# Kernel optimization log

Hardware: AMD Instinct MI355X
Metric: run time of the kernel (lower is better)

Reference implementation:

```python
import jax, jax.numpy as jnp
import numpy as np
import math

NUM_EXPERTS = 8
CAP_FACTOR = 1.25
MIN_CAPACITY = 4

def _capacity(num_tokens, num_experts):
    cap = math.floor(CAP_FACTOR * num_tokens / num_experts)
    cap += cap % 2
    return max(cap, MIN_CAPACITY)

def setup_inputs() -> dict:
    key = jax.random.key(0)
    k1, k2, k3, k4 = jax.random.split(key, 4)
    tokens, d_model, d_ff, E = 8192, 1024, 4096, NUM_EXPERTS
    x = jax.random.normal(k1, (tokens, d_model), dtype=jnp.float32)
    gate_weight = jax.random.normal(k2, (E, d_model), dtype=jnp.float32) * math.sqrt(0.1 / d_model)
    expert_weight = jax.random.normal(k3, (E, d_model, d_ff), dtype=jnp.float32) * 0.02
    expert_bias = jax.random.normal(k4, (E, 1, d_ff), dtype=jnp.float32) * 0.02
    return {"x": x, "gate_weight": gate_weight, "expert_weight": expert_weight, "expert_bias": expert_bias}

def reference(x, gate_weight, expert_weight, expert_bias):
    tokens, d_model = x.shape
    E = gate_weight.shape[0]
    capacity = _capacity(tokens, E)
    # FP32 gate (Switch-style)
    gate_logits = jnp.dot(x.astype(jnp.float32), gate_weight.astype(jnp.float32).T)  # [s, E]
    logits = jax.nn.softmax(gate_logits, axis=-1)  # auto_cast_softmax in fp32
    # Top-1 routing, select_policy='first'
    top1_idx = jnp.argmax(gate_logits, axis=-1)  # argmax over raw gate output
    mask = jax.nn.one_hot(top1_idx, E, dtype=jnp.int32)  # [s, E]
    # aux load-balancing loss (training path)
    me = jnp.mean(logits, axis=0)
    ce = jnp.mean(mask.astype(jnp.float32), axis=0)
    l_aux = E * jnp.sum(me * ce)
    # cumsum-based capacity ranking
    ranks = jnp.cumsum(mask, axis=0) - 1  # [s, E]
    mask = mask * (ranks < capacity).astype(jnp.int32)
    ranks_tok = jnp.sum(mask * ranks, axis=-1)  # [s]
    rank_oh = jax.nn.one_hot(ranks_tok, capacity, dtype=logits.dtype)  # [s, c]
    weight = mask.astype(logits.dtype) * logits  # [s, E]
    combine_weights = weight[:, :, None] * rank_oh[:, None, :]  # [s, E, c]
    sec_mask = combine_weights != 0  # bool dispatch mask
    # scatter dispatch: [s,E,c] x [s,d] -> [E,c,d]
    dispatched = jnp.einsum("sec,sd->ecd", sec_mask.astype(x.dtype), x)
    # per-expert front linear: [E,c,d] x [E,d,f] -> [E,c,f]
    out = jnp.einsum("ecd,edf->ecf", dispatched, expert_weight) + expert_bias
    return out, combine_weights, l_aux
```

## Files before the change

kernel.cpp:

```cpp
#include <hip/hip_runtime.h>
#include <hip/hip_bf16.h>

#define TOKENS 8192
#define DM 1024
#define DFF 4096
#define NE 8
#define CAP 1280
#define ECAP (NE*CAP)
#define OUT_ELEMS ((size_t)NE*CAP*DFF)
#define CMB_ELEMS ((size_t)TOKENS*NE*CAP)
#define ZROW TOKENS
#define GBK 32

typedef __attribute__((ext_vector_type(8))) short short8;
typedef __attribute__((ext_vector_type(16))) float f32x16;
typedef __attribute__((ext_vector_type(4))) float f4;

__device__ inline ushort f2bf(float f) {
    __hip_bfloat16 h = __float2bfloat16(f);
    return *reinterpret_cast<ushort*>(&h);
}

__device__ __forceinline__ void gload16(const ushort* g, short* l) {
    __builtin_amdgcn_global_load_lds(
        (const __attribute__((address_space(1))) void*)g,
        (__attribute__((address_space(3))) void*)l, 16, 0, 0);
}

__global__ __launch_bounds__(256) void gate_kernel(const float* __restrict__ x,
        const float* __restrict__ gw, float* __restrict__ probs8, int* __restrict__ top1,
        ushort* __restrict__ xbf) {
    int wave = threadIdx.x >> 6;
    int lane = threadIdx.x & 63;
    int t = blockIdx.x * 4 + wave;
    const float* xrow = x + (size_t)t * DM;
    float4 xv[4];
    #pragma unroll
    for (int j = 0; j < 4; ++j) xv[j] = *(const float4*)(xrow + lane * 4 + j * 256);
    ushort* xbrow = xbf + (size_t)t * DM;
    #pragma unroll
    for (int j = 0; j < 4; ++j) {
        ushort4 o;
        o.x = f2bf(xv[j].x); o.y = f2bf(xv[j].y); o.z = f2bf(xv[j].z); o.w = f2bf(xv[j].w);
        *(ushort4*)(xbrow + lane * 4 + j * 256) = o;
    }
    float logit[8];
    #pragma unroll
    for (int e = 0; e < 8; ++e) {
        const float* g = gw + e * DM;
        float s = 0.f;
        #pragma unroll
        for (int j = 0; j < 4; ++j) {
            float4 gv = *(const float4*)(g + lane * 4 + j * 256);
            s += xv[j].x * gv.x + xv[j].y * gv.y + xv[j].z * gv.z + xv[j].w * gv.w;
        }
        #pragma unroll
        for (int off = 32; off >= 1; off >>= 1) s += __shfl_xor(s, off);
        logit[e] = s;
    }
    if (lane == 0) {
        int bi = 0; float bv = logit[0];
        #pragma unroll
        for (int e = 1; e < 8; ++e) if (logit[e] > bv) { bv = logit[e]; bi = e; }
        float se = 0.f, p[8];
        #pragma unroll
        for (int e = 0; e < 8; ++e) { p[e] = expf(logit[e] - bv); se += p[e]; }
        float inv = 1.f / se;
        #pragma unroll
        for (int e = 0; e < 8; ++e) probs8[t * 8 + e] = p[e] * inv;
        top1[t] = bi;
    }
    if (blockIdx.x == 0) {
        ushort4 z; z.x = z.y = z.z = z.w = 0;
        *(ushort4*)(xbf + (size_t)ZROW * DM + threadIdx.x * 4) = z;
    }
}

__global__ __launch_bounds__(512) void cvtw_rank_kernel(
        const float* __restrict__ w, ushort* __restrict__ wt,
        const int* __restrict__ top1, const float* __restrict__ probs8,
        int* __restrict__ slot_token, int* __restrict__ pos,
        int* __restrict__ cnts, float* __restrict__ laux_out) {
    __shared__ __align__(16) char smem[TOKENS * 4 + 64 * 4 + 8 * 4];
    const int tid = threadIdx.x;
    if (blockIdx.x == 0) {
        int* t1s = (int*)smem;
        float* red = (float*)(smem + TOKENS * 4);
        int* cnt_sh = (int*)(smem + TOKENS * 4 + 64 * 4);
        int w8 = tid >> 6;
        int lane = tid & 63;
        for (int i = tid; i < TOKENS; i += 512) t1s[i] = top1[i];
        for (int i = tid; i < ECAP; i += 512) slot_token[i] = ZROW;
        for (int i = tid; i < TOKENS; i += 512) pos[i] = -1;

        float ps[8];
        #pragma unroll
        for (int e = 0; e < 8; ++e) ps[e] = 0.f;
        for (int t = tid; t < TOKENS; t += 512) {
            float4 a = *(const float4*)(probs8 + t * 8);
            float4 b = *(const float4*)(probs8 + t * 8 + 4);
            ps[0] += a.x; ps[1] += a.y; ps[2] += a.z; ps[3] += a.w;
            ps[4] += b.x; ps[5] += b.y; ps[6] += b.z; ps[7] += b.w;
        }
        #pragma unroll
        for (int e = 0; e < 8; ++e) {
            #pragma unroll
            for (int off = 32; off >= 1; off >>= 1) ps[e] += __shfl_xor(ps[e], off);
        }
        if (lane == 0) {
            #pragma unroll
            for (int e = 0; e < 8; ++e) red[w8 * 8 + e] = ps[e];
        }
        __syncthreads();

        int base = 0;
        for (int t0 = 0; t0 < TOKENS; t0 += 256) {
            #pragma unroll
            for (int q = 0; q < 4; ++q) {
                int t = t0 + q * 64 + lane;
                bool mine = (t1s[t] == w8);
                unsigned long long m = __ballot(mine);
                if (mine) {
                    int r = base + __popcll(m & ((1ull << lane) - 1ull));
                    if (r < CAP) { slot_token[w8 * CAP + r] = t; pos[t] = w8 * CAP + r; }
                }
                base += __popcll(m);
            }
        }
        if (lane == 0) { cnt_sh[w8] = base; cnts[w8] = (base < CAP) ? base : CAP; }
        __syncthreads();
        if (tid == 0) {
            float la = 0.f;
            #pragma unroll
            for (int e = 0; e < 8; ++e) {
                float me = 0.f;
                #pragma unroll
                for (int wv = 0; wv < 8; ++wv) me += red[wv * 8 + e];
                la += (me / (float)TOKENS) * ((float)cnt_sh[e] / (float)TOKENS);
            }
            laux_out[0] = la * (float)NE;
        }
        return;
    }
    float (*tile)[65] = (float(*)[65])smem;
    int b = blockIdx.x - 1;
    int e = b >> 11;
    int rem = b & 2047;
    int n0 = (rem & 63) * 64;
    int k0 = (rem >> 6) * 32;
    const float* we = w + (size_t)e * DM * DFF;
    int c = tid & 63, r0 = tid >> 6;
    #pragma unroll
    for (int i = 0; i < 4; ++i) {
        int r = r0 + i * 8;
        tile[r][c] = we[(size_t)(k0 + r) * DFF + n0 + c];
    }
    __syncthreads();
    ushort* wte = wt + (size_t)e * DFF * DM;
    int kc = tid & 31, nr0 = tid >> 5;
    #pragma unroll
    for (int i = 0; i < 4; ++i) {
        int nr = nr0 + i * 16;
        wte[(size_t)(n0 + nr) * DM + k0 + kc] = f2bf(tile[kc][nr]);
    }
}

__global__ __launch_bounds__(1024, 4) void gemm_kernel(
    const ushort* __restrict__ xbf,
    const ushort* __restrict__ wt,
    const float*  __restrict__ bias,
    const int*    __restrict__ slot_token,
    const int*    __restrict__ cnts,
    float* __restrict__ out,
    const int*    __restrict__ pos,
    const float*  __restrict__ probs8,
    float* __restrict__ cmb,
    int do_combine)
{
    const int bid = blockIdx.x;
    const int e   = bid & 7;
    const int rem = bid >> 3;
    const int nt  = rem & 15;
    const int mt  = rem >> 4;
    __shared__ __align__(16) short lds[4][16384];
    const int tid  = threadIdx.x;
    const int lane = tid & 63;
    const int wave = tid >> 6;
    const int wr = wave >> 2;
    const int wc = wave & 3;
    const int ln31 = lane & 31, lh = lane >> 5;
    const int tbeg = bid * 16;
    const bool has_cmb = do_combine && (bid < 512);

    float* orow = out + ((size_t)(e * CAP + mt * 256)) * DFF + (size_t)nt * 256;

    if (mt * 256 >= cnts[e]) {
        int c4 = tid & 63;
        int r0b = tid >> 6;
        f4 bv4 = *(const f4*)(bias + e * DFF + nt * 256 + c4 * 4);
        for (int r = r0b; r < 256; r += 16)
            __builtin_nontemporal_store(bv4, (f4*)(orow + (size_t)r * DFF + c4 * 4));
        if (has_cmb) {
            for (int i = 0; i < 16; ++i) {
                int tok = tbeg + i;
                int p = pos[tok];
                int ee = (p < 0) ? 0 : (p / CAP);
                float val = probs8[tok * 8 + ee];
                f4* row = (f4*)(cmb + (size_t)tok * ECAP);
                #pragma unroll
                for (int k = 0; k < 3; ++k) {
                    int c = tid + k * 1024;
                    if (c < ECAP / 4) {
                        int b4 = c * 4;
                        f4 v;
                        v.x = (b4 + 0 == p) ? val : 0.f;
                        v.y = (b4 + 1 == p) ? val : 0.f;
                        v.z = (b4 + 2 == p) ? val : 0.f;
                        v.w = (b4 + 3 == p) ? val : 0.f;
                        __builtin_nontemporal_store(v, row + c);
                    }
                }
            }
        }
        return;
    }

    const int r0 = tid >> 2;
    const int kg = (tid & 3) ^ ((tid >> 3) & 3);
    const int tokA = slot_token[e * CAP + mt * 256 + r0];
    const ushort* aptr = xbf + (size_t)tokA * DM + kg * 8;
    const ushort* bptr = wt + ((size_t)e * DFF + (size_t)nt * 256 + r0) * DM + kg * 8;

    #define STAGE(T) do { \
        short* base_ = &lds[(T) & 3][0]; \
        size_t ko_ = (size_t)(T) * GBK; \
        gload16(aptr + ko_, base_ + tid * 8); \
        gload16(bptr + ko_, base_ + 8192 + tid * 8); \
    } while (0)

    int aoff[4], boff[4];
    #pragma unroll
    for (int s = 0; s < 2; ++s) {
        #pragma unroll
        for (int mi = 0; mi < 2; ++mi) {
            int r = wr * 64 + mi * 32 + ln31;
            int c = lh + 2 * s;
            aoff[s * 2 + mi] = (r * 4 + (c ^ ((r >> 1) & 3))) * 8;
        }
        #pragma unroll
        for (int ni = 0; ni < 2; ++ni) {
            int rn = wc * 64 + ni * 32 + ln31;
            int c = lh + 2 * s;
            boff[s * 2 + ni] = 8192 + (rn * 4 + (c ^ ((rn >> 1) & 3))) * 8;
        }
    }

    f4* cmb_p = (f4*)cmb + (size_t)tbeg * (ECAP / 4);
    int kpart = 0, ntok = 0;
    int cur_p = -1, nxt_p = -1;
    float cur_val = 0.f, nxt_val = 0.f;
    if (has_cmb) {
        cur_p = pos[tbeg];
        { int ee = (cur_p < 0) ? 0 : (cur_p / CAP); cur_val = probs8[tbeg * 8 + ee]; }
        nxt_p = pos[tbeg + 1];
        { int ee = (nxt_p < 0) ? 0 : (nxt_p / CAP); nxt_val = probs8[(tbeg + 1) * 8 + ee]; }
    }
    #define CSTORE() do { if (has_cmb) { \
        int c_ = tid + kpart * 1024; \
        if (c_ < ECAP / 4) { \
            int b4_ = c_ * 4; \
            f4 v_; \
            v_.x = (b4_ + 0 == cur_p) ? cur_val : 0.f; \
            v_.y = (b4_ + 1 == cur_p) ? cur_val : 0.f; \
            v_.z = (b4_ + 2 == cur_p) ? cur_val : 0.f; \
            v_.w = (b4_ + 3 == cur_p) ? cur_val : 0.f; \
            __builtin_nontemporal_store(v_, cmb_p + c_); \
        } \
        if (++kpart == 3) { \
            kpart = 0; cmb_p += ECAP / 4; ++ntok; \
            cur_p = nxt_p; cur_val = nxt_val; \
            if (ntok + 1 < 16) { \
                nxt_p = pos[tbeg + ntok + 1]; \
                int ee_ = (nxt_p < 0) ? 0 : (nxt_p / CAP); \
                nxt_val = probs8[(tbeg + ntok + 1) * 8 + ee_]; \
            } \
        } \
    } } while (0)

    f32x16 acc[2][2];
    #pragma unroll
    for (int mi = 0; mi < 2; ++mi)
        #pragma unroll
        for (int ni = 0; ni < 2; ++ni)
            acc[mi][ni] = (f32x16)(0.f);

    STAGE(0); STAGE(1); STAGE(2);
    for (int t = 0; t < 32; ++t) {
        if (t < 29) {
            STAGE(t + 3);
            asm volatile("s_waitcnt vmcnt(6)" ::: "memory");
        } else if (t == 29) {
            asm volatile("s_waitcnt vmcnt(4)" ::: "memory");
        } else if (t == 30) {
            asm volatile("s_waitcnt vmcnt(2)" ::: "memory");
        } else {
            asm volatile("s_waitcnt vmcnt(0)" ::: "memory");
        }
        __builtin_amdgcn_s_barrier();
        __builtin_amdgcn_sched_barrier(0);

        const short* L = &lds[t & 3][0];
        __builtin_amdgcn_s_setprio(1);
        #pragma unroll
        for (int s = 0; s < 2; ++s) {
            short8 af[2], bfr[2];
            #pragma unroll
            for (int ni = 0; ni < 2; ++ni) bfr[ni] = *(const short8*)(L + boff[s * 2 + ni]);
            #pragma unroll
            for (int mi = 0; mi < 2; ++mi) af[mi] = *(const short8*)(L + aoff[s * 2 + mi]);
            #pragma unroll
            for (int mi = 0; mi < 2; ++mi)
                #pragma unroll
                for (int ni = 0; ni < 2; ++ni)
                    acc[mi][ni] = __builtin_amdgcn_mfma_f32_32x32x16_bf16(af[mi], bfr[ni], acc[mi][ni], 0, 0, 0);
        }
        __builtin_amdgcn_s_setprio(0);
        CSTORE();
        if (t < 16) CSTORE();
        __builtin_amdgcn_sched_barrier(0);
        asm volatile("" ::: "memory");
        __builtin_amdgcn_s_barrier();
        asm volatile("" ::: "memory");
    }
    #undef STAGE
    #undef CSTORE

    #pragma unroll
    for (int ni = 0; ni < 2; ++ni) {
        int c = wc * 64 + ni * 32 + ln31;
        float bv = bias[e * DFF + nt * 256 + c];
        #pragma unroll
        for (int mi = 0; mi < 2; ++mi) {
            #pragma unroll
            for (int reg = 0; reg < 16; ++reg) {
                int r = wr * 64 + mi * 32 + (reg & 3) + 8 * (reg >> 2) + 4 * lh;
                __builtin_nontemporal_store(acc[mi][ni][reg] + bv,
                    orow + (size_t)r * DFF + c);
            }
        }
    }
}

__global__ __launch_bounds__(256) void combine_kernel(const int* __restrict__ pos,
        const float* __restrict__ probs8, float* __restrict__ cmb) {
    int tok = blockIdx.x;
    int p = pos[tok];
    int e = p / CAP;
    float val = probs8[tok * 8 + (e < 0 ? 0 : e)];
    f4* row = (f4*)(cmb + (size_t)tok * ECAP);
    #pragma unroll
    for (int k = 0; k < 10; ++k) {
        int c = threadIdx.x + k * 256;
        int b4 = c * 4;
        f4 v;
        v.x = (b4 + 0 == p) ? val : 0.f;
        v.y = (b4 + 1 == p) ? val : 0.f;
        v.z = (b4 + 2 == p) ? val : 0.f;
        v.w = (b4 + 3 == p) ? val : 0.f;
        __builtin_nontemporal_store(v, row + c);
    }
}

extern "C" void kernel_launch(void* const* d_in, const int* in_sizes, int n_in,
                              void* d_out, int out_size, void* d_ws, size_t ws_size,
                              hipStream_t stream) {
    const float* x  = (const float*)d_in[0];
    const float* gw = (const float*)d_in[1];
    const float* ew = (const float*)d_in[2];
    const float* eb = (const float*)d_in[3];

    float* out = (float*)d_out;
    float* cmb = out + OUT_ELEMS;
    float* laux_out = cmb + CMB_ELEMS;

    float* probs8 = (float*)d_ws;
    int* top1 = (int*)(probs8 + TOKENS * 8);
    int* slot_token = top1 + TOKENS;
    int* pos = slot_token + ECAP;
    int* cnts = pos + TOKENS;

    const size_t SMALL = 1 << 20;
    const size_t WT_ELEMS_ = (size_t)NE * DFF * DM;
    const size_t XBF_ELEMS_ = (size_t)(TOKENS + 1) * DM;
    bool big_ws = ws_size >= SMALL + (WT_ELEMS_ + XBF_ELEMS_) * sizeof(ushort);
    ushort* wtbf = big_ws ? (ushort*)((char*)d_ws + SMALL) : (ushort*)cmb;
    ushort* xbf  = wtbf + WT_ELEMS_;

    gate_kernel<<<TOKENS / 4, 256, 0, stream>>>(x, gw, probs8, top1, xbf);
    cvtw_rank_kernel<<<16385, 512, 0, stream>>>(ew, wtbf, top1, probs8,
                                                slot_token, pos, cnts, laux_out);
    if (big_ws) {
        gemm_kernel<<<640, 1024, 0, stream>>>(xbf, wtbf, eb, slot_token, cnts, out,
                                              pos, probs8, cmb, 1);
    } else {
        gemm_kernel<<<640, 1024, 0, stream>>>(xbf, wtbf, eb, slot_token, cnts, out,
                                              pos, probs8, cmb, 0);
        combine_kernel<<<TOKENS, 256, 0, stream>>>(pos, probs8, cmb);
    }
}
```

Baseline: 191.5 us.

## Switch GEMM to 256x128 tiles with 512-thread blocks and triple-buffered LDS

The expert GEMM now uses 256x128 output tiles computed by 8 waves in 512-thread blocks, launched as 1280 blocks instead of 640 blocks of 1024 threads with 256x256 tiles. The LDS pipeline drops from four buffers of 32 KB to three of 24 KB, with prefetch depth 2 and separate vmcnt schedules for blocks that also write the combine tensor. Each block now writes 8 combine rows spread across the K loop and epilogue, and empty-expert tiles reuse the same store macro. This aims to improve occupancy and load balance, at the cost of lower B-tile reuse per block and more A-row loads overall.

```diff
diff --git a/kernel.cpp b/kernel.cpp
--- a/kernel.cpp
+++ b/kernel.cpp
@@ -165,7 +165,7 @@
     }
 }
 
-__global__ __launch_bounds__(1024, 4) void gemm_kernel(
+__global__ __launch_bounds__(512, 4) void gemm_kernel(
     const ushort* __restrict__ xbf,
     const ushort* __restrict__ wt,
     const float*  __restrict__ bias,
@@ -180,80 +180,19 @@
     const int bid = blockIdx.x;
     const int e   = bid & 7;
     const int rem = bid >> 3;
-    const int nt  = rem & 15;
-    const int mt  = rem >> 4;
-    __shared__ __align__(16) short lds[4][16384];
+    const int nt  = rem & 31;
+    const int mt  = rem >> 5;
+    __shared__ __align__(16) short lds[3][12288];
     const int tid  = threadIdx.x;
     const int lane = tid & 63;
     const int wave = tid >> 6;
-    const int wr = wave >> 2;
-    const int wc = wave & 3;
+    const int wr = wave >> 1;
+    const int wc = wave & 1;
     const int ln31 = lane & 31, lh = lane >> 5;
-    const int tbeg = bid * 16;
-    const bool has_cmb = do_combine && (bid < 512);
-
-    float* orow = out + ((size_t)(e * CAP + mt * 256)) * DFF + (size_t)nt * 256;
-
-    if (mt * 256 >= cnts[e]) {
-        int c4 = tid & 63;
-        int r0b = tid >> 6;
-        f4 bv4 = *(const f4*)(bias + e * DFF + nt * 256 + c4 * 4);
-        for (int r = r0b; r < 256; r += 16)
-            __builtin_nontemporal_store(bv4, (f4*)(orow + (size_t)r * DFF + c4 * 4));
-        if (has_cmb) {
-            for (int i = 0; i < 16; ++i) {
-                int tok = tbeg + i;
-                int p = pos[tok];
-                int ee = (p < 0) ? 0 : (p / CAP);
-                float val = probs8[tok * 8 + ee];
-                f4* row = (f4*)(cmb + (size_t)tok * ECAP);
-                #pragma unroll
-                for (int k = 0; k < 3; ++k) {
-                    int c = tid + k * 1024;
-                    if (c < ECAP / 4) {
-                        int b4 = c * 4;
-                        f4 v;
-                        v.x = (b4 + 0 == p) ? val : 0.f;
-                        v.y = (b4 + 1 == p) ? val : 0.f;
-                        v.z = (b4 + 2 == p) ? val : 0.f;
-                        v.w = (b4 + 3 == p) ? val : 0.f;
-                        __builtin_nontemporal_store(v, row + c);
-                    }
-                }
-            }
-        }
-        return;
-    }
-
-    const int r0 = tid >> 2;
-    const int kg = (tid & 3) ^ ((tid >> 3) & 3);
-    const int tokA = slot_token[e * CAP + mt * 256 + r0];
-    const ushort* aptr = xbf + (size_t)tokA * DM + kg * 8;
-    const ushort* bptr = wt + ((size_t)e * DFF + (size_t)nt * 256 + r0) * DM + kg * 8;
-
-    #define STAGE(T) do { \
-        short* base_ = &lds[(T) & 3][0]; \
-        size_t ko_ = (size_t)(T) * GBK; \
-        gload16(aptr + ko_, base_ + tid * 8); \
-        gload16(bptr + ko_, base_ + 8192 + tid * 8); \
-    } while (0)
-
-    int aoff[4], boff[4];
-    #pragma unroll
-    for (int s = 0; s < 2; ++s) {
-        #pragma unroll
-        for (int mi = 0; mi < 2; ++mi) {
-            int r = wr * 64 + mi * 32 + ln31;
-            int c = lh + 2 * s;
-            aoff[s * 2 + mi] = (r * 4 + (c ^ ((r >> 1) & 3))) * 8;
-        }
-        #pragma unroll
-        for (int ni = 0; ni < 2; ++ni) {
-            int rn = wc * 64 + ni * 32 + ln31;
-            int c = lh + 2 * s;
-            boff[s * 2 + ni] = 8192 + (rn * 4 + (c ^ ((rn >> 1) & 3))) * 8;
-        }
-    }
+    const int tbeg = bid * 8;
+    const bool has_cmb = do_combine && (bid < 1024);
+
+    float* orow = out + ((size_t)(e * CAP + mt * 256)) * DFF + (size_t)nt * 128;
 
     f4* cmb_p = (f4*)cmb + (size_t)tbeg * (ECAP / 4);
     int kpart = 0, ntok = 0;
@@ -265,27 +204,68 @@
         nxt_p = pos[tbeg + 1];
         { int ee = (nxt_p < 0) ? 0 : (nxt_p / CAP); nxt_val = probs8[(tbeg + 1) * 8 + ee]; }
     }
-    #define CSTORE() do { if (has_cmb) { \
-        int c_ = tid + kpart * 1024; \
-        if (c_ < ECAP / 4) { \
-            int b4_ = c_ * 4; \
-            f4 v_; \
-            v_.x = (b4_ + 0 == cur_p) ? cur_val : 0.f; \
-            v_.y = (b4_ + 1 == cur_p) ? cur_val : 0.f; \
-            v_.z = (b4_ + 2 == cur_p) ? cur_val : 0.f; \
-            v_.w = (b4_ + 3 == cur_p) ? cur_val : 0.f; \
-            __builtin_nontemporal_store(v_, cmb_p + c_); \
-        } \
-        if (++kpart == 3) { \
+    #define CSTORE() do { \
+        int c_ = tid + kpart * 512; \
+        int b4_ = c_ * 4; \
+        f4 v_; \
+        v_.x = (b4_ + 0 == cur_p) ? cur_val : 0.f; \
+        v_.y = (b4_ + 1 == cur_p) ? cur_val : 0.f; \
+        v_.z = (b4_ + 2 == cur_p) ? cur_val : 0.f; \
+        v_.w = (b4_ + 3 == cur_p) ? cur_val : 0.f; \
+        __builtin_nontemporal_store(v_, cmb_p + c_); \
+        if (++kpart == 5) { \
             kpart = 0; cmb_p += ECAP / 4; ++ntok; \
             cur_p = nxt_p; cur_val = nxt_val; \
-            if (ntok + 1 < 16) { \
+            if (ntok + 1 < 8) { \
                 nxt_p = pos[tbeg + ntok + 1]; \
                 int ee_ = (nxt_p < 0) ? 0 : (nxt_p / CAP); \
                 nxt_val = probs8[(tbeg + ntok + 1) * 8 + ee_]; \
             } \
         } \
-    } } while (0)
+    } while (0)
+
+    if (mt * 256 >= cnts[e]) {
+        int c4 = tid & 31;
+        int r0b = tid >> 5;
+        f4 bv4 = *(const f4*)(bias + e * DFF + nt * 128 + c4 * 4);
+        for (int r = r0b; r < 256; r += 16)
+            __builtin_nontemporal_store(bv4, (f4*)(orow + (size_t)r * DFF + c4 * 4));
+        if (has_cmb) { while (ntok < 8) CSTORE(); }
+        return;
+    }
+
+    const int r0a = tid >> 2;
+    const int kg = (tid & 3) ^ ((tid >> 3) & 3);
+    const int tokA0 = slot_token[e * CAP + mt * 256 + r0a];
+    const int tokA1 = slot_token[e * CAP + mt * 256 + 128 + r0a];
+    const ushort* aptr0 = xbf + (size_t)tokA0 * DM + kg * 8;
+    const ushort* aptr1 = xbf + (size_t)tokA1 * DM + kg * 8;
+    const ushort* bptr  = wt + ((size_t)e * DFF + (size_t)nt * 128 + r0a) * DM + kg * 8;
+
+    #define STAGE(T, BUF) do { \
+        short* base_ = &lds[BUF][0]; \
+        size_t ko_ = (size_t)(T) * GBK; \
+        gload16(aptr0 + ko_, base_ + tid * 8); \
+        gload16(aptr1 + ko_, base_ + 4096 + tid * 8); \
+        gload16(bptr  + ko_, base_ + 8192 + tid * 8); \
+    } while (0)
+
+    int aoff[4], boff[4];
+    #pragma unroll
+    for (int s = 0; s < 2; ++s) {
+        #pragma unroll
+        for (int mi = 0; mi < 2; ++mi) {
+            int r = wr * 64 + mi * 32 + ln31;
+            int c = lh + 2 * s;
+            aoff[s * 2 + mi] = (r * 4 + (c ^ ((r >> 1) & 3))) * 8;
+        }
+        #pragma unroll
+        for (int ni = 0; ni < 2; ++ni) {
+            int rn = wc * 64 + ni * 32 + ln31;
+            int c = lh + 2 * s;
+            boff[s * 2 + ni] = 8192 + (rn * 4 + (c ^ ((rn >> 1) & 3))) * 8;
+        }
+    }
 
     f32x16 acc[2][2];
     #pragma unroll
@@ -294,51 +274,58 @@
         for (int ni = 0; ni < 2; ++ni)
             acc[mi][ni] = (f32x16)(0.f);
 
-    STAGE(0); STAGE(1); STAGE(2);
-    for (int t = 0; t < 32; ++t) {
-        if (t < 29) {
-            STAGE(t + 3);
-            asm volatile("s_waitcnt vmcnt(6)" ::: "memory");
-        } else if (t == 29) {
-            asm volatile("s_waitcnt vmcnt(4)" ::: "memory");
-        } else if (t == 30) {
-            asm volatile("s_waitcnt vmcnt(2)" ::: "memory");
-        } else {
-            asm volatile("s_waitcnt vmcnt(0)" ::: "memory");
-        }
-        __builtin_amdgcn_s_barrier();
-        __builtin_amdgcn_sched_barrier(0);
-
-        const short* L = &lds[t & 3][0];
-        __builtin_amdgcn_s_setprio(1);
-        #pragma unroll
-        for (int s = 0; s < 2; ++s) {
-            short8 af[2], bfr[2];
-            #pragma unroll
-            for (int ni = 0; ni < 2; ++ni) bfr[ni] = *(const short8*)(L + boff[s * 2 + ni]);
-            #pragma unroll
-            for (int mi = 0; mi < 2; ++mi) af[mi] = *(const short8*)(L + aoff[s * 2 + mi]);
-            #pragma unroll
-            for (int mi = 0; mi < 2; ++mi)
-                #pragma unroll
-                for (int ni = 0; ni < 2; ++ni)
-                    acc[mi][ni] = __builtin_amdgcn_mfma_f32_32x32x16_bf16(af[mi], bfr[ni], acc[mi][ni], 0, 0, 0);
-        }
-        __builtin_amdgcn_s_setprio(0);
-        CSTORE();
-        if (t < 16) CSTORE();
-        __builtin_amdgcn_sched_barrier(0);
-        asm volatile("" ::: "memory");
-        __builtin_amdgcn_s_barrier();
-        asm volatile("" ::: "memory");
-    }
+    STAGE(0, 0); STAGE(1, 1);
+    int cur = 0;
+    int nxt2 = 2;
+    #define KLOOP(W0, W1, WS, W30, W31, DOCMB) \
+    for (int t = 0; t < 32; ++t) { \
+        if (t < 30) STAGE(t + 2, nxt2); \
+        if (t == 0)       asm volatile("s_waitcnt vmcnt(" #W0 ")" ::: "memory"); \
+        else if (t == 1)  asm volatile("s_waitcnt vmcnt(" #W1 ")" ::: "memory"); \
+        else if (t < 30)  asm volatile("s_waitcnt vmcnt(" #WS ")" ::: "memory"); \
+        else if (t == 30) asm volatile("s_waitcnt vmcnt(" #W30 ")" ::: "memory"); \
+        else              asm volatile("s_waitcnt vmcnt(" #W31 ")" ::: "memory"); \
+        __builtin_amdgcn_s_barrier();            \
+        __builtin_amdgcn_sched_barrier(0); \
+        { \
+            const short* L = &lds[cur][0]; \
+            __builtin_amdgcn_s_setprio(1); \
+            _Pragma("unroll") \
+            for (int s = 0; s < 2; ++s) { \
+                short8 af[2], bfr[2]; \
+                _Pragma("unroll") \
+                for (int ni = 0; ni < 2; ++ni) bfr[ni] = *(const short8*)(L + boff[s * 2 + ni]); \
+                _Pragma("unroll") \
+                for (int mi = 0; mi < 2; ++mi) af[mi] = *(const short8*)(L + aoff[s * 2 + mi]); \
+                _Pragma("unroll") \
+                for (int mi = 0; mi < 2; ++mi) \
+                    _Pragma("unroll") \
+                    for (int ni = 0; ni < 2; ++ni) \
+                        acc[mi][ni] = __builtin_amdgcn_mfma_f32_32x32x16_bf16(af[mi], bfr[ni], acc[mi][ni], 0, 0, 0); \
+            } \
+            __builtin_amdgcn_s_setprio(0); \
+        } \
+        if (DOCMB) CSTORE();                     \
+        __builtin_amdgcn_sched_barrier(0); \
+        asm volatile("" ::: "memory"); \
+        __builtin_amdgcn_s_barrier();            \
+        asm volatile("" ::: "memory"); \
+        cur = (cur == 2) ? 0 : cur + 1; \
+        nxt2 = (nxt2 == 2) ? 0 : nxt2 + 1; \
+    }
+
+    if (has_cmb) {
+        KLOOP(6, 7, 8, 5, 2, 1);
+    } else {
+        KLOOP(6, 6, 6, 3, 0, 0);
+    }
+    #undef KLOOP
     #undef STAGE
-    #undef CSTORE
 
     #pragma unroll
     for (int ni = 0; ni < 2; ++ni) {
         int c = wc * 64 + ni * 32 + ln31;
-        float bv = bias[e * DFF + nt * 256 + c];
+        float bv = bias[e * DFF + nt * 128 + c];
         #pragma unroll
         for (int mi = 0; mi < 2; ++mi) {
             #pragma unroll
@@ -349,6 +336,8 @@
             }
         }
     }
+    if (has_cmb) { while (ntok < 8) CSTORE(); }
+    #undef CSTORE
 }
 
 __global__ __launch_bounds__(256) void combine_kernel(const int* __restrict__ pos,
@@ -400,10 +389,10 @@
     cvtw_rank_kernel<<<16385, 512, 0, stream>>>(ew, wtbf, top1, probs8,
                                                 slot_token, pos, cnts, laux_out);
     if (big_ws) {
-        gemm_kernel<<<640, 1024, 0, stream>>>(xbf, wtbf, eb, slot_token, cnts, out,
+        gemm_kernel<<<1280, 512, 0, stream>>>(xbf, wtbf, eb, slot_token, cnts, out,
                                               pos, probs8, cmb, 1);
     } else {
-        gemm_kernel<<<640, 1024, 0, stream>>>(xbf, wtbf, eb, slot_token, cnts, out,
+        gemm_kernel<<<1280, 512, 0, stream>>>(xbf, wtbf, eb, slot_token, cnts, out,
                                               pos, probs8, cmb, 0);
         combine_kernel<<<TOKENS, 256, 0, stream>>>(pos, probs8, cmb);
     }
```

Measured after the change: 187.5 us (median of 4 runs). 1.02x faster.
